# Kernel optimization log

Hardware: AMD Instinct MI355X
Metric: run time of the kernel (lower is better)

Reference implementation:

```python
import jax, jax.numpy as jnp
import numpy as np

MAX_TRAV = 21  # matches the torch module constant


def setup_inputs() -> dict:
    key = jax.random.key(0)
    k1, _ = jax.random.split(key)
    B, H, W = 4, 2048, 2048
    untraversable = jax.random.randint(k1, (B, H, W), 0, 2).astype(jnp.bool_)
    max_sq = jnp.ones((1,), dtype=jnp.float32) * float(MAX_TRAV ** 2)  # 441.0
    return {"untraversable": untraversable, "max_sq": max_sq}


def _chamfer(untraversable, max_sq):
    big = max_sq[0]
    B, H, W = untraversable.shape
    # 0 at obstacles, MAX_TRAV^2 elsewhere (values are small exact ints in fp32)
    sq = jnp.where(untraversable, jnp.float32(0.0), big)
    # odd increments 1,3,...,41: cumulative sum of first k odds = k^2
    ds = jnp.arange(1, 2 * MAX_TRAV + 1, 2, dtype=jnp.float32)

    col = jnp.full((B, H, 1), big, dtype=jnp.float32)

    def hstep(s, d):
        from_right = jnp.concatenate([s[:, :, 1:] + d, col], axis=2)
        from_left = jnp.concatenate([col, s[:, :, :-1] + d], axis=2)
        return jnp.minimum(s, jnp.minimum(from_right, from_left)), None

    sq, _ = jax.lax.scan(hstep, sq, ds)

    row = jnp.full((B, 1, W), big, dtype=jnp.float32)

    def vstep(s, d):
        from_below = jnp.concatenate([s[:, 1:, :] + d, row], axis=1)
        from_above = jnp.concatenate([row, s[:, :-1, :] + d], axis=1)
        return jnp.minimum(s, jnp.minimum(from_below, from_above)), None

    sq, _ = jax.lax.scan(vstep, sq, ds)
    return jnp.sqrt(sq)


def reference(untraversable, max_sq):
    return _chamfer(untraversable, max_sq)
```

## Files before the change

### kernel.cpp

```cpp
#include <hip/hip_runtime.h>
#include <cstdint>

#define BB 4
#define HH 2048
#define WW 2048
#define MAXT 21
#define BIGSQ 441

__global__ __launch_bounds__(256) void hpass(const int* __restrict__ in,
                                             uint8_t* __restrict__ dh) {
    const int tid  = threadIdx.x;
    const int lane = tid & 63;
    const int w    = tid >> 6;
    const int row  = blockIdx.x;
    const long long ro = (long long)row * WW;
    const int x0   = w << 9;

    int v[8];
    #pragma unroll
    for (int j = 0; j < 8; ++j)
        v[j] = in[ro + x0 + (j << 6) + lane];

    unsigned long long b[10];
    b[0] = 0; b[9] = 0;
    if (x0 > 0)
        b[0] = __ballot(in[ro + x0 - 64 + lane] != 0);
    if (x0 + 512 < WW)
        b[9] = __ballot(in[ro + x0 + 512 + lane] != 0);
    #pragma unroll
    for (int j = 0; j < 8; ++j)
        b[j + 1] = __ballot(v[j] != 0);

    #pragma unroll
    for (int j = 0; j < 8; ++j) {
        const unsigned long long mc = b[j + 1];
        unsigned long long right = mc >> lane;
        if (lane) right |= b[j + 2] << (64 - lane);
        unsigned long long left = mc << (63 - lane);
        if (lane != 63) left |= b[j] >> (lane + 1);

        int dr = right ? __builtin_ctzll(right) : 64;
        int dl = left  ? __builtin_clzll(left)  : 64;
        int d  = min(min(dr, dl), MAXT);
        dh[ro + x0 + (j << 6) + lane] = (uint8_t)d;
    }
}

__global__ __launch_bounds__(256) void vpass(const uint8_t* __restrict__ dh,
                                             float* __restrict__ out) {
    __shared__ uint16_t s[106][64];
    const int tid = threadIdx.x;
    const int x0  = blockIdx.x << 6;
    const int y0  = blockIdx.y << 6;
    const int b   = blockIdx.z;
    const long long base = (long long)b * HH * WW;

    for (int i = tid; i < 106 * 16; i += 256) {
        int r  = i >> 4;
        int c4 = (i & 15) << 2;
        int gy = y0 - 21 + r;
        ushort4 val;
        if (gy >= 0 && gy < HH) {
            const uint8_t* p = dh + base + (long long)gy * WW + x0 + c4;
            uchar4 u = *(const uchar4*)p;
            val.x = (uint16_t)(u.x * u.x);
            val.y = (uint16_t)(u.y * u.y);
            val.z = (uint16_t)(u.z * u.z);
            val.w = (uint16_t)(u.w * u.w);
        } else {
            val.x = val.y = val.z = val.w = BIGSQ;
        }
        *(ushort4*)&s[r][c4] = val;
    }
    __syncthreads();

    const int c  = tid & 63;
    const int j0 = (tid >> 6) << 4;
    for (int k = 0; k < 16; ++k) {
        const int j  = j0 + k;
        const int yl = 21 + j;
        int val = s[yl][c];
        for (int d = 1; d <= MAXT; ++d) {
            const int dd = d * d;
            if (__all(dd >= val)) break;
            int t1 = s[yl - d][c] + dd;
            int t2 = s[yl + d][c] + dd;
            val = min(val, min(t1, t2));
        }
        out[base + (long long)(y0 + j) * WW + x0 + c] = sqrtf((float)val);
    }
}

extern "C" void kernel_launch(void* const* d_in, const int* in_sizes, int n_in,
                              void* d_out, int out_size, void* d_ws, size_t ws_size,
                              hipStream_t stream) {
    const int* unt = (const int*)d_in[0];
    uint8_t* dh    = (uint8_t*)d_ws;
    float* out     = (float*)d_out;

    hpass<<<dim3(BB * HH), 256, 0, stream>>>(unt, dh);
    vpass<<<dim3(WW / 64, HH / 64, BB), 256, 0, stream>>>(dh, out);
}
```

Before: 45.90 us.

## Widen vertical-pass tiles to 128 columns and process four columns per thread

The vertical pass now covers a 128-column tile per block. Each thread handles four adjacent columns using packed 16-bit values in 32-bit registers (SWAR add) and 8-byte LDS reads, then writes its outputs as one float4 store. This cuts the number of LDS instructions and global stores per output and halves the grid size. The early-exit test now uses the max of four columns across the wave, which may run more iterations, and fewer blocks lowers occupancy.

Measured after the change: 41.46 us. 9.7% less time.

```diff
diff --git a/kernel.cpp b/kernel.cpp
--- a/kernel.cpp
+++ b/kernel.cpp
@@ -6,6 +6,8 @@
 #define WW 2048
 #define MAXT 21
 #define BIGSQ 441
+
+static __device__ __forceinline__ uint32_t umin32(uint32_t a, uint32_t b) { return a < b ? a : b; }
 
 __global__ __launch_bounds__(256) void hpass(const int* __restrict__ in,
                                              uint8_t* __restrict__ dh) {
@@ -48,46 +50,70 @@
 
 __global__ __launch_bounds__(256) void vpass(const uint8_t* __restrict__ dh,
                                              float* __restrict__ out) {
-    __shared__ uint16_t s[106][64];
+    __shared__ uint16_t s[106][128];
     const int tid = threadIdx.x;
-    const int x0  = blockIdx.x << 6;
+    const int x0  = blockIdx.x << 7;
     const int y0  = blockIdx.y << 6;
     const int b   = blockIdx.z;
     const long long base = (long long)b * HH * WW;
 
     for (int i = tid; i < 106 * 16; i += 256) {
         int r  = i >> 4;
-        int c4 = (i & 15) << 2;
+        int c8 = (i & 15) << 3;
         int gy = y0 - 21 + r;
-        ushort4 val;
+        uint4 pk;
         if (gy >= 0 && gy < HH) {
-            const uint8_t* p = dh + base + (long long)gy * WW + x0 + c4;
-            uchar4 u = *(const uchar4*)p;
-            val.x = (uint16_t)(u.x * u.x);
-            val.y = (uint16_t)(u.y * u.y);
-            val.z = (uint16_t)(u.z * u.z);
-            val.w = (uint16_t)(u.w * u.w);
+            const uint8_t* p = dh + base + (long long)gy * WW + x0 + c8;
+            uint2 u = *(const uint2*)p;
+            uint32_t e0 = u.x & 0xff, e1 = (u.x >> 8) & 0xff, e2 = (u.x >> 16) & 0xff, e3 = u.x >> 24;
+            uint32_t e4 = u.y & 0xff, e5 = (u.y >> 8) & 0xff, e6 = (u.y >> 16) & 0xff, e7 = u.y >> 24;
+            pk.x = (e0 * e0) | ((e1 * e1) << 16);
+            pk.y = (e2 * e2) | ((e3 * e3) << 16);
+            pk.z = (e4 * e4) | ((e5 * e5) << 16);
+            pk.w = (e6 * e6) | ((e7 * e7) << 16);
         } else {
-            val.x = val.y = val.z = val.w = BIGSQ;
+            pk.x = pk.y = pk.z = pk.w = BIGSQ | (BIGSQ << 16);
         }
-        *(ushort4*)&s[r][c4] = val;
+        *(uint4*)&s[r][c8] = pk;
     }
     __syncthreads();
 
-    const int c  = tid & 63;
-    const int j0 = (tid >> 6) << 4;
-    for (int k = 0; k < 16; ++k) {
-        const int j  = j0 + k;
+    const int lane = tid & 63;
+    const int w    = tid >> 6;
+    const int cg   = (lane & 31) << 2;
+    const int ro   = lane >> 5;
+    for (int k = 0; k < 8; ++k) {
+        const int j  = (w << 4) + (k << 1) + ro;
         const int yl = 21 + j;
-        int val = s[yl][c];
+
+        uint2 q = *(const uint2*)&s[yl][cg];
+        uint32_t v0 = q.x & 0xffff, v1 = q.x >> 16;
+        uint32_t v2 = q.y & 0xffff, v3 = q.y >> 16;
+
         for (int d = 1; d <= MAXT; ++d) {
-            const int dd = d * d;
-            if (__all(dd >= val)) break;
-            int t1 = s[yl - d][c] + dd;
-            int t2 = s[yl + d][c] + dd;
-            val = min(val, min(t1, t2));
+            const uint32_t dd = (uint32_t)(d * d);
+            uint32_t h = umin32(0, 0);
+            h = v0 > v1 ? v0 : v1;
+            uint32_t h2 = v2 > v3 ? v2 : v3;
+            h = h > h2 ? h : h2;
+            if (__all(dd >= h)) break;
+            uint2 a  = *(const uint2*)&s[yl - d][cg];
+            uint2 bq = *(const uint2*)&s[yl + d][cg];
+            const uint32_t dd2 = dd * 0x10001u;
+            uint32_t A0 = a.x + dd2, A1 = a.y + dd2;
+            uint32_t B0 = bq.x + dd2, B1 = bq.y + dd2;
+            v0 = umin32(v0, umin32(A0 & 0xffff, B0 & 0xffff));
+            v1 = umin32(v1, umin32(A0 >> 16,    B0 >> 16));
+            v2 = umin32(v2, umin32(A1 & 0xffff, B1 & 0xffff));
+            v3 = umin32(v3, umin32(A1 >> 16,    B1 >> 16));
         }
-        out[base + (long long)(y0 + j) * WW + x0 + c] = sqrtf((float)val);
+
+        float4 o;
+        o.x = sqrtf((float)v0);
+        o.y = sqrtf((float)v1);
+        o.z = sqrtf((float)v2);
+        o.w = sqrtf((float)v3);
+        *(float4*)&out[base + (long long)(y0 + j) * WW + x0 + cg] = o;
     }
 }
 
@@ -99,5 +125,5 @@
     float* out     = (float*)d_out;
 
     hpass<<<dim3(BB * HH), 256, 0, stream>>>(unt, dh);
-    vpass<<<dim3(WW / 64, HH / 64, BB), 256, 0, stream>>>(dh, out);
+    vpass<<<dim3(WW / 128, HH / 64, BB), 256, 0, stream>>>(dh, out);
 }
```
